# Performance work log

Measured on AMD Instinct MI355X. Metric: run time of the kernel, lower is better.

## Reference

```python
import jax, jax.numpy as jnp
import numpy as np
import math

EMB_DIM = 256
HEADS = 8
HEAD_DIM = EMB_DIM // HEADS
N_LAYERS = 6
GRID_H = 32
GRID_W = 32
SEQ = GRID_H * GRID_W
LN_EPS = 1e-5


def _layernorm(x, w, b):
    mu = jnp.mean(x, axis=-1, keepdims=True)
    var = jnp.mean(jnp.square(x - mu), axis=-1, keepdims=True)
    return (x - mu) * jax.lax.rsqrt(var + LN_EPS) * w + b


def _sinusoidal_table(num_pos, dim):
    inv_freq = 1.0 / (10000.0 ** (jnp.arange(0, dim, 2, dtype=jnp.float32) / dim))
    t = jnp.arange(num_pos, dtype=jnp.float32)
    sinusoid = t[:, None] * inv_freq[None, :]  # [P, dim/2]
    return jnp.concatenate([jnp.sin(sinusoid), jnp.cos(sinusoid)], axis=-1)  # [P, dim]


def _alibi_bias(num_heads, seq_len):
    # 2D Manhattan distances over the flattened grid (Two-slope-Alibi: factors = 1)
    xs, ys = jnp.meshgrid(jnp.arange(GRID_H), jnp.arange(GRID_W), indexing='ij')
    xf = xs.reshape(-1).astype(jnp.float32)
    yf = ys.reshape(-1).astype(jnp.float32)
    dist = jnp.abs(xf[:, None] - xf[None, :]) + jnp.abs(yf[:, None] - yf[None, :])
    dist = jnp.abs(dist[:seq_len, :seq_len])  # rpe_abs=True
    i = jnp.arange(num_heads, dtype=jnp.float32)
    slopes_l = -(2.0 ** (-(1.0 + i)))   # start_exponent=1, geometric ratio 1/2, times -1
    slopes_r = -(2.0 ** (-(0.5 + i)))   # start_exponent=0.5
    alibi_l = slopes_l[:, None, None] * dist[None]
    alibi_r = slopes_r[:, None, None] * dist[None]
    # triu + tril (diagonal dist = 0 so double-count is harmless)
    return jnp.triu(alibi_r) + jnp.tril(alibi_l)  # [H, S, S]


def reference(tokens, pos_ids, emb_table, input_weight, position_weight,
              ln1_w, ln1_b, ln2_w, ln2_b, w1, b1, w2, b2, lnf_w, lnf_b):
    B, S = tokens.shape
    # embeddings + sinusoidal positional embedding, mixed via weighted_sum_no_norm
    x_emb = emb_table[tokens]                                   # [B, S, D]
    pos_emb = _sinusoidal_table(SEQ, EMB_DIM)[pos_ids][None]    # [1, S, D]
    x = input_weight * x_emb + position_weight * pos_emb        # [B, S, D]

    bias = _alibi_bias(HEADS, S)[None]                          # [1, H, S, S]
    scale = 1.0 / math.sqrt(HEAD_DIM)

    for l in range(N_LAYERS):
        # --- attention: manual 2D-Alibi path (q = k = v = layernormed x; no projections) ---
        xn = _layernorm(x, ln1_w[l], ln1_b[l])
        qkv = xn.reshape(B, S, HEADS, HEAD_DIM).transpose(0, 2, 1, 3)  # [B, H, S, d]
        scores = jnp.einsum('bhsd,bhtd->bhst', qkv, qkv) * scale + bias
        attn = jax.nn.softmax(scores, axis=-1)
        out = jnp.einsum('bhst,bhtd->bhsd', attn, qkv)
        out = out.transpose(0, 2, 1, 3).reshape(B, S, EMB_DIM)
        x = x + out
        # --- MLP: Linear(D, 2*mlp_dim) -> GELU(exact) -> Linear(2*mlp_dim, D) ---
        xn = _layernorm(x, ln2_w[l], ln2_b[l])
        h = jax.nn.gelu(xn @ w1[l] + b1[l], approximate=False)
        x = x + (h @ w2[l] + b2[l])

    return _layernorm(x, lnf_w, lnf_b)


def setup_inputs() -> dict:
    key = jax.random.key(0)
    ks = jax.random.split(key, 8)
    B, S, D, L = 16, SEQ, EMB_DIM, N_LAYERS
    H2 = 2 * 512  # mlp hidden = mlp_dim * 2
    return {
        'tokens': jax.random.randint(ks[0], (B, S), 0, 16),
        'pos_ids': jnp.arange(S),
        'emb_table': jax.random.normal(ks[1], (16, D), dtype=jnp.float32),
        'input_weight': jnp.ones((1,), jnp.float32),
        'position_weight': jnp.ones((1,), jnp.float32),
        'ln1_w': jnp.ones((L, D), jnp.float32),
        'ln1_b': jnp.zeros((L, D), jnp.float32),
        'ln2_w': jnp.ones((L, D), jnp.float32),
        'ln2_b': jnp.zeros((L, D), jnp.float32),
        'w1': jax.random.normal(ks[2], (L, D, H2), dtype=jnp.float32) * (1.0 / np.sqrt(D)),
        'b1': jnp.zeros((L, H2), jnp.float32),
        'w2': jax.random.normal(ks[3], (L, H2, D), dtype=jnp.float32) * (1.0 / np.sqrt(H2)),
        'b2': jnp.zeros((L, D), jnp.float32),
        'lnf_w': jnp.ones((D,), jnp.float32),
        'lnf_b': jnp.zeros((D,), jnp.float32),
    }
```

## Files before the change

### kernel.cpp

```cpp
#include <hip/hip_runtime.h>
#include <hip/hip_bf16.h>
#include <math.h>

#define B_   16
#define S_   1024
#define D_   256
#define H_   8
#define HD_  32
#define L_   6
#define H2_  1024
#define LN_EPS 1e-5f
#define LOG2E_ 1.4426950408889634f
#define SCALE_ 0.17677669529663687f

typedef __attribute__((ext_vector_type(8))) short frag;
typedef __attribute__((ext_vector_type(4))) float f32x4;

#define MFMA(a, b, c) __builtin_amdgcn_mfma_f32_16x16x32_bf16((a), (b), (c), 0, 0, 0)

__device__ inline ushort bf16b(float f) {
    uint u = __builtin_bit_cast(uint, f);
    u += 0x7fff + ((u >> 16) & 1);
    return (ushort)(u >> 16);
}
__device__ inline uint cvt_pk_bf16(float lo, float hi) {
    uint r;
    asm("v_cvt_pk_bf16_f32 %0, %1, %2" : "=v"(r) : "v"(lo), "v"(hi));
    return r;
}
__device__ inline float exp2_raw(float x) {
    float r;
    asm("v_exp_f32 %0, %1" : "=v"(r) : "v"(x));
    return r;
}
__device__ __forceinline__ void gload16(const ushort* g, ushort* l) {
    __builtin_amdgcn_global_load_lds(
        (const __attribute__((address_space(1))) uint*)g,
        (__attribute__((address_space(3))) uint*)l, 16, 0, 0);
}

__global__ __launch_bounds__(256) void wtr_kernel(
    const float* __restrict__ in, ushort* __restrict__ out, int K, int N)
{
    __shared__ ushort Ts[32][36];
    in  += (size_t)blockIdx.z * K * N;
    out += (size_t)blockIdx.z * K * N;
    int n0 = blockIdx.x * 32, k0 = blockIdx.y * 32;
    int r = threadIdx.x >> 3, c4 = (threadIdx.x & 7) * 4;
    float4 f = *(const float4*)(in + (size_t)(k0 + r) * N + n0 + c4);
    Ts[r][c4 + 0] = bf16b(f.x);
    Ts[r][c4 + 1] = bf16b(f.y);
    Ts[r][c4 + 2] = bf16b(f.z);
    Ts[r][c4 + 3] = bf16b(f.w);
    __syncthreads();
    ushort4 o = { Ts[c4 + 0][r], Ts[c4 + 1][r], Ts[c4 + 2][r], Ts[c4 + 3][r] };
    *(ushort4*)(out + (size_t)(n0 + r) * K + k0 + c4) = o;
}

__global__ __launch_bounds__(256) void embed_kernel(
    const int* __restrict__ tokens, const int* __restrict__ pos_ids,
    const float* __restrict__ emb, const float* __restrict__ iwp,
    const float* __restrict__ pwp, float* __restrict__ X)
{
    int bs = blockIdx.x;
    int s = bs & (S_ - 1);
    int d = threadIdx.x;
    int tok = tokens[bs];
    float p = (float)pos_ids[s];
    int j = (d < 128) ? d : (d - 128);
    float invf = exp2f(-(float)j * (13.287712379549449f / 128.0f));
    float ang = p * invf;
    float pe = (d < 128) ? sinf(ang) : cosf(ang);
    X[(size_t)bs * D_ + d] = iwp[0] * emb[tok * D_ + d] + pwp[0] * pe;
}

template<int MODE>
__global__ __launch_bounds__(256) void ln_kernel(
    const float* __restrict__ X, const float* __restrict__ w,
    const float* __restrict__ b, void* __restrict__ outp)
{
    int row = blockIdx.x * 4 + (threadIdx.x >> 6);
    int lane = threadIdx.x & 63;
    const float4 v = *(const float4*)(X + (size_t)row * D_ + lane * 4);
    float s = v.x + v.y + v.z + v.w;
    #pragma unroll
    for (int m = 1; m < 64; m <<= 1) s += __shfl_xor(s, m, 64);
    float mu = s * (1.0f / 256.0f);
    float dx = v.x - mu, dy = v.y - mu, dz = v.z - mu, dw = v.w - mu;
    float vs = dx * dx + dy * dy + dz * dz + dw * dw;
    #pragma unroll
    for (int m = 1; m < 64; m <<= 1) vs += __shfl_xor(vs, m, 64);
    float inv = rsqrtf(vs * (1.0f / 256.0f) + LN_EPS);
    float4 wv = *(const float4*)(w + lane * 4);
    float4 bv = *(const float4*)(b + lane * 4);
    float o0 = dx * inv * wv.x + bv.x;
    float o1 = dy * inv * wv.y + bv.y;
    float o2 = dz * inv * wv.z + bv.z;
    float o3 = dw * inv * wv.w + bv.w;
    if constexpr (MODE == 0) {
        float4 o = { o0, o1, o2, o3 };
        *(float4*)((float*)outp + (size_t)row * D_ + lane * 4) = o;
    } else if constexpr (MODE == 1) {
        int bb = row >> 10, ss = row & 1023;
        int h = lane >> 3, dd = (lane & 7) * 4;
        ushort4 o = { bf16b(o0), bf16b(o1), bf16b(o2), bf16b(o3) };
        *(ushort4*)((ushort*)outp + (((size_t)(bb * H_ + h) * S_ + ss) * HD_ + dd)) = o;
    } else {
        ushort4 o = { bf16b(o0), bf16b(o1), bf16b(o2), bf16b(o3) };
        *(ushort4*)((ushort*)outp + (size_t)row * D_ + lane * 4) = o;
    }
}

__global__ __launch_bounds__(256) void vtr_kernel(
    const ushort* __restrict__ XNB, ushort* __restrict__ VTI)
{
    __shared__ ushort Ts[32][136];
    const int bh = blockIdx.y;
    const int sblk = blockIdx.x * 128;
    const ushort* __restrict__ base = XNB + (size_t)bh * (S_ * HD_);
    #pragma unroll
    for (int i = 0; i < 2; ++i) {
        int cid = i * 256 + threadIdx.x;
        int s = cid >> 2, c = cid & 3;
        uint4 u = *(const uint4*)(base + (size_t)(sblk + s) * HD_ + c * 8);
        int col = (s & ~63) + 32 * ((s >> 4) & 1) + 8 * ((s >> 2) & 3)
                + 4 * ((s >> 5) & 1) + (s & 3);
        int d0 = c * 8;
        Ts[d0 + 0][col] = (ushort)(u.x & 0xffff);
        Ts[d0 + 1][col] = (ushort)(u.x >> 16);
        Ts[d0 + 2][col] = (ushort)(u.y & 0xffff);
        Ts[d0 + 3][col] = (ushort)(u.y >> 16);
        Ts[d0 + 4][col] = (ushort)(u.z & 0xffff);
        Ts[d0 + 5][col] = (ushort)(u.z >> 16);
        Ts[d0 + 6][col] = (ushort)(u.w & 0xffff);
        Ts[d0 + 7][col] = (ushort)(u.w >> 16);
    }
    __syncthreads();
    #pragma unroll
    for (int i = 0; i < 2; ++i) {
        int cid = i * 256 + threadIdx.x;
        int d = cid >> 4, ch = cid & 15;
        uint4 o = *(const uint4*)&Ts[d][ch * 8];
        *(uint4*)(VTI + ((size_t)bh * HD_ + d) * S_ + sblk + ch * 8) = o;
    }
}

__global__ __launch_bounds__(256) void attn_kernel(
    const ushort* __restrict__ XNB, const ushort* __restrict__ VTI,
    float* __restrict__ X)
{
    const int bi = blockIdx.x;
    const int xcd = bi & 7, m = bi >> 3;
    const int bh = xcd * 16 + (m >> 3);
    const int bx = m & 7;
    const int b = bh >> 3, h = bh & 7;

    const ushort* __restrict__ base = XNB + (size_t)bh * (S_ * HD_);
    const ushort* __restrict__ vbase = VTI + (size_t)bh * (HD_ * S_);
    const int tid = threadIdx.x;
    const int w = tid >> 6, l = tid & 63, g = l >> 4, ll = l & 15;
    const int q0 = bx * 128 + w * 32;
    const int qgA = q0 + ll, qgB = q0 + 16 + ll;
    const int xq = q0 >> 5;
    const int yqA = ll, yqB = 16 + ll;

    const float C1 = SCALE_ * LOG2E_;
    frag qfA = *(const frag*)(base + (size_t)qgA * HD_ + g * 8);
    frag qfB = *(const frag*)(base + (size_t)qgB * HD_ + g * 8);
    #pragma unroll
    for (int i = 0; i < 8; ++i) {
        float fa = __builtin_bit_cast(float, ((uint)(ushort)qfA[i]) << 16);
        float fb = __builtin_bit_cast(float, ((uint)(ushort)qfB[i]) << 16);
        qfA[i] = (short)bf16b(fa * C1);
        qfB[i] = (short)bf16b(fb * C1);
    }

    const float slr = -exp2f(-(0.5f + (float)h)) * LOG2E_;
    const float sll = -exp2f(-(1.0f + (float)h)) * LOG2E_;
    const int itb = 2 * bx + (w >> 1);

    float dabs[4], d16m[4], d16p[4];
    #pragma unroll
    for (int r = 0; r < 4; ++r) {
        int del = ll - 4 * g - r;
        dabs[r] = (float)abs(del);
        d16m[r] = (float)(16 - del);
        d16p[r] = (float)(16 + del);
    }

    f32x4 o0A = {0,0,0,0}, o1A = {0,0,0,0}, osA = {0,0,0,0};
    f32x4 o0B = {0,0,0,0}, o1B = {0,0,0,0}, osB = {0,0,0,0};
    const f32x4 zc = {0,0,0,0};
    const short one_s = (short)0x3F80;
    const frag ones = { one_s, one_s, one_s, one_s, one_s, one_s, one_s, one_s };

    const ushort* kp  = base  + (size_t)ll * HD_ + g * 8;
    const ushort* vpa = vbase + (size_t)ll * S_ + g * 8;
    const ushort* vpb = vbase + (size_t)(16 + ll) * S_ + g * 8;

    frag Ka0, Ka1, Ka2, Ka3, Va0, Va1, Va2, Va3;
    frag Kb0, Kb1, Kb2, Kb3, Vb0, Vb1, Vb2, Vb3;

    Ka0 = *(const frag*)(kp);
    Ka1 = *(const frag*)(kp + 16 * HD_);
    Ka2 = *(const frag*)(kp + 32 * HD_);
    Ka3 = *(const frag*)(kp + 48 * HD_);
    Va0 = *(const frag*)(vpa);
    Va1 = *(const frag*)(vpb);
    Va2 = *(const frag*)(vpa + 32);
    Va3 = *(const frag*)(vpb + 32);
    kp += 64 * HD_; vpa += 64; vpb += 64;

#define EXACTR(r)                                                             \
  { int t0 = tb + 4 * g + (r);                                                \
    { int tg = t0;      int xt = tg >> 5, yt = tg & 31;                       \
      eA0[r] = exp2_raw(fmaf((tg > qgA) ? slr : sll,                          \
               (float)(abs(xq - xt) + abs(yqA - yt)), sa0[r]));               \
      eB0[r] = exp2_raw(fmaf((tg > qgB) ? slr : sll,                          \
               (float)(abs(xq - xt) + abs(yqB - yt)), sb0[r])); }             \
    { int tg = t0 + 16; int xt = tg >> 5, yt = tg & 31;                       \
      eA1[r] = exp2_raw(fmaf((tg > qgA) ? slr : sll,                          \
               (float)(abs(xq - xt) + abs(yqA - yt)), sa1[r]));               \
      eB1[r] = exp2_raw(fmaf((tg > qgB) ? slr : sll,                          \
               (float)(abs(xq - xt) + abs(yqB - yt)), sb1[r])); }             \
    { int tg = t0 + 32; int xt = tg >> 5, yt = tg & 31;                       \
      eA2[r] = exp2_raw(fmaf((tg > qgA) ? slr : sll,                          \
               (float)(abs(xq - xt) + abs(yqA - yt)), sa2[r]));               \
      eB2[r] = exp2_raw(fmaf((tg > qgB) ? slr : sll,                          \
               (float)(abs(xq - xt) + abs(yqB - yt)), sb2[r])); }             \
    { int tg = t0 + 48; int xt = tg >> 5, yt = tg & 31;                       \
      eA3[r] = exp2_raw(fmaf((tg > qgA) ? slr : sll,                          \
               (float)(abs(xq - xt) + abs(yqA - yt)), sa3[r]));               \
      eB3[r] = exp2_raw(fmaf((tg > qgB) ? slr : sll,                          \
               (float)(abs(xq - xt) + abs(yqB - yt)), sb3[r])); } }

#define FASTR(r)                                                              \
    eA0[r] = exp2_raw(fmaf(sl, dabs[r] + ax0, sa0[r]));                       \
    eA1[r] = exp2_raw(fmaf(sl, d16m[r] + ax0, sa1[r]));                       \
    eA2[r] = exp2_raw(fmaf(sl, dabs[r] + ax1, sa2[r]));                       \
    eA3[r] = exp2_raw(fmaf(sl, d16m[r] + ax1, sa3[r]));                       \
    eB0[r] = exp2_raw(fmaf(sl, d16p[r] + ax0, sb0[r]));                       \
    eB1[r] = exp2_raw(fmaf(sl, dabs[r] + ax0, sb1[r]));                       \
    eB2[r] = exp2_raw(fmaf(sl, d16p[r] + ax1, sb2[r]));                       \
    eB3[r] = exp2_raw(fmaf(sl, dabs[r] + ax1, sb3[r]));

#define STEP(IT, K0,K1,K2,K3, V0,V1,V2,V3, NK0,NK1,NK2,NK3, NV0,NV1,NV2,NV3) \
  { NK0 = *(const frag*)(kp);                                                 \
    NK1 = *(const frag*)(kp + 16 * HD_);                                      \
    NK2 = *(const frag*)(kp + 32 * HD_);                                      \
    NK3 = *(const frag*)(kp + 48 * HD_);                                      \
    NV0 = *(const frag*)(vpa);                                                \
    NV1 = *(const frag*)(vpb);                                                \
    NV2 = *(const frag*)(vpa + 32);                                           \
    NV3 = *(const frag*)(vpb + 32);                                           \
    kp += 64 * HD_; vpa += 64; vpb += 64;                                     \
    const int tb = (IT) * 64;                                                 \
    __builtin_amdgcn_s_setprio(1);                                            \
    f32x4 sa0 = MFMA(K0, qfA, zc);                                            \
    f32x4 sa1 = MFMA(K1, qfA, zc);                                            \
    f32x4 sa2 = MFMA(K2, qfA, zc);                                            \
    f32x4 sa3 = MFMA(K3, qfA, zc);                                            \
    f32x4 sb0 = MFMA(K0, qfB, zc);                                            \
    f32x4 sb1 = MFMA(K1, qfB, zc);                                            \
    f32x4 sb2 = MFMA(K2, qfB, zc);                                            \
    f32x4 sb3 = MFMA(K3, qfB, zc);                                            \
    __builtin_amdgcn_s_setprio(0);                                            \
    f32x4 eA0, eA1, eA2, eA3, eB0, eB1, eB2, eB3;                             \
    if ((IT) == itb) {                                                        \
        EXACTR(0) EXACTR(1) EXACTR(2) EXACTR(3)                               \
    } else {                                                                  \
        const float sl = ((IT) > itb) ? slr : sll;                            \
        const float ax0 = (float)abs(xq - 2 * (IT));                          \
        const float ax1 = (float)abs(xq - 2 * (IT) - 1);                      \
        FASTR(0) FASTR(1) FASTR(2) FASTR(3)                                   \
    }                                                                         \
    uint4 pa0 = { cvt_pk_bf16(eA0[0], eA0[1]), cvt_pk_bf16(eA0[2], eA0[3]),   \
                  cvt_pk_bf16(eA2[0], eA2[1]), cvt_pk_bf16(eA2[2], eA2[3]) }; \
    uint4 pa1 = { cvt_pk_bf16(eA1[0], eA1[1]), cvt_pk_bf16(eA1[2], eA1[3]),   \
                  cvt_pk_bf16(eA3[0], eA3[1]), cvt_pk_bf16(eA3[2], eA3[3]) }; \
    uint4 pb0 = { cvt_pk_bf16(eB0[0], eB0[1]), cvt_pk_bf16(eB0[2], eB0[3]),   \
                  cvt_pk_bf16(eB2[0], eB2[1]), cvt_pk_bf16(eB2[2], eB2[3]) }; \
    uint4 pb1 = { cvt_pk_bf16(eB1[0], eB1[1]), cvt_pk_bf16(eB1[2], eB1[3]),   \
                  cvt_pk_bf16(eB3[0], eB3[1]), cvt_pk_bf16(eB3[2], eB3[3]) }; \
    frag pfA0 = __builtin_bit_cast(frag, pa0);                                \
    frag pfA1 = __builtin_bit_cast(frag, pa1);                                \
    frag pfB0 = __builtin_bit_cast(frag, pb0);                                \
    frag pfB1 = __builtin_bit_cast(frag, pb1);                                \
    __builtin_amdgcn_s_setprio(1);                                            \
    o0A = MFMA(pfA0, V0, o0A);  o1A = MFMA(pfA0, V1, o1A);                    \
    osA = MFMA(pfA0, ones, osA);                                              \
    o0A = MFMA(pfA1, V2, o0A);  o1A = MFMA(pfA1, V3, o1A);                    \
    osA = MFMA(pfA1, ones, osA);                                              \
    o0B = MFMA(pfB0, V0, o0B);  o1B = MFMA(pfB0, V1, o1B);                    \
    osB = MFMA(pfB0, ones, osB);                                              \
    o0B = MFMA(pfB1, V2, o0B);  o1B = MFMA(pfB1, V3, o1B);                    \
    osB = MFMA(pfB1, ones, osB);                                              \
    __builtin_amdgcn_s_setprio(0);                                            \
  }

    for (int it2 = 0; it2 < 16; it2 += 2) {
        STEP(it2,     Ka0,Ka1,Ka2,Ka3, Va0,Va1,Va2,Va3,
                      Kb0,Kb1,Kb2,Kb3, Vb0,Vb1,Vb2,Vb3)
        STEP(it2 + 1, Kb0,Kb1,Kb2,Kb3, Vb0,Vb1,Vb2,Vb3,
                      Ka0,Ka1,Ka2,Ka3, Va0,Va1,Va2,Va3)
    }
#undef STEP
#undef FASTR
#undef EXACTR

    #pragma unroll
    for (int r = 0; r < 4; ++r) {
        float invA = 1.0f / osA[r];
        float invB = 1.0f / osB[r];
        float* xpA = X + ((size_t)(b * S_ + q0 + g * 4 + r)) * D_ + h * HD_;
        float* xpB = X + ((size_t)(b * S_ + q0 + 16 + g * 4 + r)) * D_ + h * HD_;
        xpA[ll]      += o0A[r] * invA;
        xpA[16 + ll] += o1A[r] * invA;
        xpB[ll]      += o0B[r] * invB;
        xpB[16 + ll] += o1B[r] * invB;
    }
}

__global__ __launch_bounds__(256) void gemm1_kernel(
    const ushort* __restrict__ A, const ushort* __restrict__ Bt,
    const float* __restrict__ bias, ushort* __restrict__ Hout)
{
    __shared__ ushort As[128 * 32];
    __shared__ ushort Bs[128 * 32];
    const int tid = threadIdx.x;
    const int w = tid >> 6, l = tid & 63, g = l >> 4, ll = l & 15;
    const int wm = w >> 1, wn = w & 1;
    const int row0 = blockIdx.y * 128, col0 = blockIdx.x * 128;

    const int srow = w * 32 + (l >> 2);
    const int scol = (l & 3) * 8;
    const ushort* ga = A  + (size_t)(row0 + srow) * 256 + scol;
    const ushort* gb = Bt + (size_t)(col0 + srow) * 256 + scol;
    ushort* lA = &As[w * 1024 + l * 8];
    ushort* lB = &Bs[w * 1024 + l * 8];

    f32x4 acc[4][4] = {};
    for (int k0 = 0; k0 < 256; k0 += 32) {
        __syncthreads();
        gload16(ga + k0,            lA);
        gload16(ga + k0 + 16 * 256, lA + 512);
        gload16(gb + k0,            lB);
        gload16(gb + k0 + 16 * 256, lB + 512);
        __syncthreads();
        frag af[4], bfr[4];
        #pragma unroll
        for (int mb = 0; mb < 4; ++mb)
            af[mb] = *(const frag*)&As[(wm * 64 + mb * 16 + ll) * 32 + g * 8];
        #pragma unroll
        for (int nb = 0; nb < 4; ++nb)
            bfr[nb] = *(const frag*)&Bs[(wn * 64 + nb * 16 + ll) * 32 + g * 8];
        #pragma unroll
        for (int mb = 0; mb < 4; ++mb)
            #pragma unroll
            for (int nb = 0; nb < 4; ++nb)
                acc[mb][nb] = MFMA(af[mb], bfr[nb], acc[mb][nb]);
    }

    #pragma unroll
    for (int nb = 0; nb < 4; ++nb) {
        int col = col0 + wn * 64 + nb * 16 + ll;
        float bv = bias[col];
        #pragma unroll
        for (int mb = 0; mb < 4; ++mb) {
            #pragma unroll
            for (int r = 0; r < 4; ++r) {
                int row = row0 + wm * 64 + mb * 16 + g * 4 + r;
                float v = acc[mb][nb][r] + bv;
                float u2 = 1.5957691216f * v + 0.0713548162f * (v * v * v);
                float e = exp2_raw(u2 * LOG2E_);
                float rr = __builtin_amdgcn_rcpf(e + 1.0f);
                float gl = v - v * rr;
                Hout[(size_t)row * 1024 + col] = bf16b(gl);
            }
        }
    }
}

__global__ __launch_bounds__(256) void gemm2_kernel(
    const ushort* __restrict__ A, const ushort* __restrict__ Bt,
    const float* __restrict__ bias, float* __restrict__ X)
{
    __shared__ ushort As[128 * 32];
    __shared__ ushort Bs[64 * 32];
    const int tid = threadIdx.x;
    const int w = tid >> 6, l = tid & 63, g = l >> 4, ll = l & 15;
    const int row0 = blockIdx.y * 128, col0 = blockIdx.x * 64;

    const int srow = w * 32 + (l >> 2);
    const int scol = (l & 3) * 8;
    const ushort* ga = A  + (size_t)(row0 + srow) * 1024 + scol;
    const ushort* gb = Bt + (size_t)(col0 + w * 16 + (l >> 2)) * 1024 + scol;
    ushort* lA = &As[w * 1024 + l * 8];
    ushort* lB = &Bs[w * 512 + l * 8];

    f32x4 acc[2][4] = {};
    for (int k0 = 0; k0 < 1024; k0 += 32) {
        __syncthreads();
        gload16(ga + k0,             lA);
        gload16(ga + k0 + 16 * 1024, lA + 512);
        gload16(gb + k0,             lB);
        __syncthreads();
        frag af[2], bfr[4];
        #pragma unroll
        for (int mb = 0; mb < 2; ++mb)
            af[mb] = *(const frag*)&As[(w * 32 + mb * 16 + ll) * 32 + g * 8];
        #pragma unroll
        for (int nb = 0; nb < 4; ++nb)
            bfr[nb] = *(const frag*)&Bs[(nb * 16 + ll) * 32 + g * 8];
        #pragma unroll
        for (int mb = 0; mb < 2; ++mb)
            #pragma unroll
            for (int nb = 0; nb < 4; ++nb)
                acc[mb][nb] = MFMA(af[mb], bfr[nb], acc[mb][nb]);
    }

    #pragma unroll
    for (int nb = 0; nb < 4; ++nb) {
        int col = col0 + nb * 16 + ll;
        float bv = bias[col];
        #pragma unroll
        for (int mb = 0; mb < 2; ++mb) {
            #pragma unroll
            for (int r = 0; r < 4; ++r) {
                int row = row0 + w * 32 + mb * 16 + g * 4 + r;
                float* xp = X + (size_t)row * 256 + col;
                *xp += acc[mb][nb][r] + bv;
            }
        }
    }
}

extern "C" void kernel_launch(void* const* d_in, const int* in_sizes, int n_in,
                              void* d_out, int out_size, void* d_ws, size_t ws_size,
                              hipStream_t stream)
{
    const int*   tokens  = (const int*)d_in[0];
    const int*   pos_ids = (const int*)d_in[1];
    const float* emb     = (const float*)d_in[2];
    const float* iw      = (const float*)d_in[3];
    const float* pw      = (const float*)d_in[4];
    const float* ln1w    = (const float*)d_in[5];
    const float* ln1b    = (const float*)d_in[6];
    const float* ln2w    = (const float*)d_in[7];
    const float* ln2b    = (const float*)d_in[8];
    const float* w1      = (const float*)d_in[9];
    const float* b1      = (const float*)d_in[10];
    const float* w2      = (const float*)d_in[11];
    const float* b2      = (const float*)d_in[12];
    const float* lnfw    = (const float*)d_in[13];
    const float* lnfb    = (const float*)d_in[14];

    float* x = (float*)d_out;
    char* ws = (char*)d_ws;
    ushort* xn   = (ushort*)ws;
    ushort* vti  = (ushort*)(ws + 8388608);
    ushort* hbuf = (ushort*)(ws + 16777216);
    ushort* w1t  = (ushort*)(ws + 50331648);
    ushort* w2t  = (ushort*)(ws + 53477376);

    wtr_kernel<<<dim3(32, 8, L_), 256, 0, stream>>>(w1, w1t, 256, 1024);
    wtr_kernel<<<dim3(8, 32, L_), 256, 0, stream>>>(w2, w2t, 1024, 256);

    embed_kernel<<<B_ * S_, 256, 0, stream>>>(tokens, pos_ids, emb, iw, pw, x);

    for (int l = 0; l < L_; l++) {
        ln_kernel<1><<<(B_ * S_) / 4, 256, 0, stream>>>(x, ln1w + l * D_, ln1b + l * D_, xn);
        vtr_kernel<<<dim3(S_ / 128, B_ * H_), 256, 0, stream>>>(xn, vti);
        attn_kernel<<<(S_ / 128) * B_ * H_, 256, 0, stream>>>(xn, vti, x);
        ln_kernel<2><<<(B_ * S_) / 4, 256, 0, stream>>>(x, ln2w + l * D_, ln2b + l * D_, xn);
        gemm1_kernel<<<dim3(H2_ / 128, (B_ * S_) / 128), 256, 0, stream>>>(
            xn, w1t + (size_t)l * D_ * H2_, b1 + (size_t)l * H2_, hbuf);
        gemm2_kernel<<<dim3(D_ / 64, (B_ * S_) / 128), 256, 0, stream>>>(
            hbuf, w2t + (size_t)l * H2_ * D_, b2 + (size_t)l * D_, x);
    }
    ln_kernel<0><<<(B_ * S_) / 4, 256, 0, stream>>>(x, lnfw, lnfb, x);
}
```

Before: 730.6 us.

## Stage attention K/V tiles through double-buffered LDS instead of per-wave global loads

The attention kernel now cooperatively loads each 64-key K and V tile into double-buffered shared memory, using async global-to-LDS copies (gload16), and each wave reads its fragments from LDS. Before, every wave loaded the same K/V fragments straight from global memory into registers. The aim is to cut redundant global/L2 traffic, since four waves share one tile. The cost is a block-wide barrier every iteration, and the s_setprio hints around the MFMAs are dropped. gload16 is assumed to be defined in the part of the file not shown.

```diff
diff --git a/kernel.cpp b/kernel.cpp
--- a/kernel.cpp
+++ b/kernel.cpp
@@ -149,6 +149,9 @@
     const ushort* __restrict__ XNB, const ushort* __restrict__ VTI,
     float* __restrict__ X)
 {
+    __shared__ ushort Kl[2][2048];
+    __shared__ ushort Vl[2][2048];
+
     const int bi = blockIdx.x;
     const int xcd = bi & 7, m = bi >> 3;
     const int bh = xcd * 16 + (m >> 3);
@@ -194,22 +197,16 @@
     const short one_s = (short)0x3F80;
     const frag ones = { one_s, one_s, one_s, one_s, one_s, one_s, one_s, one_s };
 
-    const ushort* kp  = base  + (size_t)ll * HD_ + g * 8;
-    const ushort* vpa = vbase + (size_t)ll * S_ + g * 8;
-    const ushort* vpb = vbase + (size_t)(16 + ll) * S_ + g * 8;
-
-    frag Ka0, Ka1, Ka2, Ka3, Va0, Va1, Va2, Va3;
-    frag Kb0, Kb1, Kb2, Kb3, Vb0, Vb1, Vb2, Vb3;
-
-    Ka0 = *(const frag*)(kp);
-    Ka1 = *(const frag*)(kp + 16 * HD_);
-    Ka2 = *(const frag*)(kp + 32 * HD_);
-    Ka3 = *(const frag*)(kp + 48 * HD_);
-    Va0 = *(const frag*)(vpa);
-    Va1 = *(const frag*)(vpb);
-    Va2 = *(const frag*)(vpa + 32);
-    Va3 = *(const frag*)(vpb + 32);
-    kp += 64 * HD_; vpa += 64; vpb += 64;
+    const ushort* ksrc = base  + (size_t)(16 * w + ll) * HD_ + g * 8;
+    const ushort* vsrc = vbase + (size_t)((w >> 1) * 16 + ll) * S_ + (w & 1) * 32 + g * 8;
+    const int dst = (w * 64 + l) * 8;
+
+#define STAGE(NB, TILE)                                                       \
+    gload16(ksrc + (size_t)(TILE) * 64 * HD_, &Kl[NB][dst]);                  \
+    gload16(vsrc + (TILE) * 64,               &Vl[NB][dst]);
+
+    STAGE(0, 0)
+    __syncthreads();
 
 #define EXACTR(r)                                                             \
   { int t0 = tb + 4 * g + (r);                                                \
@@ -244,67 +241,63 @@
     eB2[r] = exp2_raw(fmaf(sl, d16p[r] + ax1, sb2[r]));                       \
     eB3[r] = exp2_raw(fmaf(sl, dabs[r] + ax1, sb3[r]));
 
-#define STEP(IT, K0,K1,K2,K3, V0,V1,V2,V3, NK0,NK1,NK2,NK3, NV0,NV1,NV2,NV3) \
-  { NK0 = *(const frag*)(kp);                                                 \
-    NK1 = *(const frag*)(kp + 16 * HD_);                                      \
-    NK2 = *(const frag*)(kp + 32 * HD_);                                      \
-    NK3 = *(const frag*)(kp + 48 * HD_);                                      \
-    NV0 = *(const frag*)(vpa);                                                \
-    NV1 = *(const frag*)(vpb);                                                \
-    NV2 = *(const frag*)(vpa + 32);                                           \
-    NV3 = *(const frag*)(vpb + 32);                                           \
-    kp += 64 * HD_; vpa += 64; vpb += 64;                                     \
-    const int tb = (IT) * 64;                                                 \
-    __builtin_amdgcn_s_setprio(1);                                            \
-    f32x4 sa0 = MFMA(K0, qfA, zc);                                            \
-    f32x4 sa1 = MFMA(K1, qfA, zc);                                            \
-    f32x4 sa2 = MFMA(K2, qfA, zc);                                            \
-    f32x4 sa3 = MFMA(K3, qfA, zc);                                            \
-    f32x4 sb0 = MFMA(K0, qfB, zc);                                            \
-    f32x4 sb1 = MFMA(K1, qfB, zc);                                            \
-    f32x4 sb2 = MFMA(K2, qfB, zc);                                            \
-    f32x4 sb3 = MFMA(K3, qfB, zc);                                            \
-    __builtin_amdgcn_s_setprio(0);                                            \
-    f32x4 eA0, eA1, eA2, eA3, eB0, eB1, eB2, eB3;                             \
-    if ((IT) == itb) {                                                        \
-        EXACTR(0) EXACTR(1) EXACTR(2) EXACTR(3)                               \
-    } else {                                                                  \
-        const float sl = ((IT) > itb) ? slr : sll;                            \
-        const float ax0 = (float)abs(xq - 2 * (IT));                          \
-        const float ax1 = (float)abs(xq - 2 * (IT) - 1);                      \
-        FASTR(0) FASTR(1) FASTR(2) FASTR(3)                                   \
-    }                                                                         \
-    uint4 pa0 = { cvt_pk_bf16(eA0[0], eA0[1]), cvt_pk_bf16(eA0[2], eA0[3]),   \
-                  cvt_pk_bf16(eA2[0], eA2[1]), cvt_pk_bf16(eA2[2], eA2[3]) }; \
-    uint4 pa1 = { cvt_pk_bf16(eA1[0], eA1[1]), cvt_pk_bf16(eA1[2], eA1[3]),   \
-                  cvt_pk_bf16(eA3[0], eA3[1]), cvt_pk_bf16(eA3[2], eA3[3]) }; \
-    uint4 pb0 = { cvt_pk_bf16(eB0[0], eB0[1]), cvt_pk_bf16(eB0[2], eB0[3]),   \
-                  cvt_pk_bf16(eB2[0], eB2[1]), cvt_pk_bf16(eB2[2], eB2[3]) }; \
-    uint4 pb1 = { cvt_pk_bf16(eB1[0], eB1[1]), cvt_pk_bf16(eB1[2], eB1[3]),   \
-                  cvt_pk_bf16(eB3[0], eB3[1]), cvt_pk_bf16(eB3[2], eB3[3]) }; \
-    frag pfA0 = __builtin_bit_cast(frag, pa0);                                \
-    frag pfA1 = __builtin_bit_cast(frag, pa1);                                \
-    frag pfB0 = __builtin_bit_cast(frag, pb0);                                \
-    frag pfB1 = __builtin_bit_cast(frag, pb1);                                \
-    __builtin_amdgcn_s_setprio(1);                                            \
-    o0A = MFMA(pfA0, V0, o0A);  o1A = MFMA(pfA0, V1, o1A);                    \
-    osA = MFMA(pfA0, ones, osA);                                              \
-    o0A = MFMA(pfA1, V2, o0A);  o1A = MFMA(pfA1, V3, o1A);                    \
-    osA = MFMA(pfA1, ones, osA);                                              \
-    o0B = MFMA(pfB0, V0, o0B);  o1B = MFMA(pfB0, V1, o1B);                    \
-    osB = MFMA(pfB0, ones, osB);                                              \
-    o0B = MFMA(pfB1, V2, o0B);  o1B = MFMA(pfB1, V3, o1B);                    \
-    osB = MFMA(pfB1, ones, osB);                                              \
-    __builtin_amdgcn_s_setprio(0);                                            \
-  }
-
-    for (int it2 = 0; it2 < 16; it2 += 2) {
-        STEP(it2,     Ka0,Ka1,Ka2,Ka3, Va0,Va1,Va2,Va3,
-                      Kb0,Kb1,Kb2,Kb3, Vb0,Vb1,Vb2,Vb3)
-        STEP(it2 + 1, Kb0,Kb1,Kb2,Kb3, Vb0,Vb1,Vb2,Vb3,
-                      Ka0,Ka1,Ka2,Ka3, Va0,Va1,Va2,Va3)
-    }
-#undef STEP
+    for (int it = 0; it < 16; ++it) {
+        const int cur = it & 1, nxt = cur ^ 1;
+        const int tb = it * 64;
+        STAGE(nxt, (it + 1) & 15)
+
+        frag K0 = *(const frag*)&Kl[cur][l * 8];
+        frag K1 = *(const frag*)&Kl[cur][512 + l * 8];
+        frag K2 = *(const frag*)&Kl[cur][1024 + l * 8];
+        frag K3 = *(const frag*)&Kl[cur][1536 + l * 8];
+        frag V0 = *(const frag*)&Vl[cur][l * 8];
+        frag V2 = *(const frag*)&Vl[cur][512 + l * 8];
+        frag V1 = *(const frag*)&Vl[cur][1024 + l * 8];
+        frag V3 = *(const frag*)&Vl[cur][1536 + l * 8];
+
+        f32x4 sa0 = MFMA(K0, qfA, zc);
+        f32x4 sa1 = MFMA(K1, qfA, zc);
+        f32x4 sa2 = MFMA(K2, qfA, zc);
+        f32x4 sa3 = MFMA(K3, qfA, zc);
+        f32x4 sb0 = MFMA(K0, qfB, zc);
+        f32x4 sb1 = MFMA(K1, qfB, zc);
+        f32x4 sb2 = MFMA(K2, qfB, zc);
+        f32x4 sb3 = MFMA(K3, qfB, zc);
+
+        f32x4 eA0, eA1, eA2, eA3, eB0, eB1, eB2, eB3;
+        if (it == itb) {
+            EXACTR(0) EXACTR(1) EXACTR(2) EXACTR(3)
+        } else {
+            const float sl = (it > itb) ? slr : sll;
+            const float ax0 = (float)abs(xq - 2 * it);
+            const float ax1 = (float)abs(xq - 2 * it - 1);
+            FASTR(0) FASTR(1) FASTR(2) FASTR(3)
+        }
+        uint4 pa0 = { cvt_pk_bf16(eA0[0], eA0[1]), cvt_pk_bf16(eA0[2], eA0[3]),
+                      cvt_pk_bf16(eA2[0], eA2[1]), cvt_pk_bf16(eA2[2], eA2[3]) };
+        uint4 pa1 = { cvt_pk_bf16(eA1[0], eA1[1]), cvt_pk_bf16(eA1[2], eA1[3]),
+                      cvt_pk_bf16(eA3[0], eA3[1]), cvt_pk_bf16(eA3[2], eA3[3]) };
+        uint4 pb0 = { cvt_pk_bf16(eB0[0], eB0[1]), cvt_pk_bf16(eB0[2], eB0[3]),
+                      cvt_pk_bf16(eB2[0], eB2[1]), cvt_pk_bf16(eB2[2], eB2[3]) };
+        uint4 pb1 = { cvt_pk_bf16(eB1[0], eB1[1]), cvt_pk_bf16(eB1[2], eB1[3]),
+                      cvt_pk_bf16(eB3[0], eB3[1]), cvt_pk_bf16(eB3[2], eB3[3]) };
+        frag pfA0 = __builtin_bit_cast(frag, pa0);
+        frag pfA1 = __builtin_bit_cast(frag, pa1);
+        frag pfB0 = __builtin_bit_cast(frag, pb0);
+        frag pfB1 = __builtin_bit_cast(frag, pb1);
+
+        o0A = MFMA(pfA0, V0, o0A);  o1A = MFMA(pfA0, V1, o1A);
+        osA = MFMA(pfA0, ones, osA);
+        o0A = MFMA(pfA1, V2, o0A);  o1A = MFMA(pfA1, V3, o1A);
+        osA = MFMA(pfA1, ones, osA);
+        o0B = MFMA(pfB0, V0, o0B);  o1B = MFMA(pfB0, V1, o1B);
+        osB = MFMA(pfB0, ones, osB);
+        o0B = MFMA(pfB1, V2, o0B);  o1B = MFMA(pfB1, V3, o1B);
+        osB = MFMA(pfB1, ones, osB);
+
+        __syncthreads();
+    }
+#undef STAGE
 #undef FASTR
 #undef EXACTR
 
```

Result: faster. 679.3 us (-7.0%).

## Stage K/V tiles through LDS triple buffer and software-pipeline QK with PV

Applied to the files above, without the earlier changes.

Replaces per-wave direct global loads of K and V fragments with cooperative async global-to-LDS loads into a three-slot ring buffer, synchronised with waitcnt and barriers. Each wave now loads one quarter of each tile instead of every wave loading the whole tile, removing redundant global traffic across the four waves. The loop is also restructured so the next tile's QK MFMAs are issued alongside the current tile's PV MFMAs, with the exp computation moved after them, so matrix and vector work can overlap. It adds a block-wide barrier every tile, LDS usage that may lower occupancy, and extra register pressure from carrying scores across iterations. The final round stages a tile index that wraps to 0 and is never used, wasting a small load.

```diff
diff --git a/kernel.cpp b/kernel.cpp
--- a/kernel.cpp
+++ b/kernel.cpp
@@ -149,6 +149,9 @@
     const ushort* __restrict__ XNB, const ushort* __restrict__ VTI,
     float* __restrict__ X)
 {
+    __shared__ ushort Kl[3][2048];
+    __shared__ ushort Vl[3][2048];
+
     const int bi = blockIdx.x;
     const int xcd = bi & 7, m = bi >> 3;
     const int bh = xcd * 16 + (m >> 3);
@@ -194,25 +197,19 @@
     const short one_s = (short)0x3F80;
     const frag ones = { one_s, one_s, one_s, one_s, one_s, one_s, one_s, one_s };
 
-    const ushort* kp  = base  + (size_t)ll * HD_ + g * 8;
-    const ushort* vpa = vbase + (size_t)ll * S_ + g * 8;
-    const ushort* vpb = vbase + (size_t)(16 + ll) * S_ + g * 8;
-
-    frag Ka0, Ka1, Ka2, Ka3, Va0, Va1, Va2, Va3;
-    frag Kb0, Kb1, Kb2, Kb3, Vb0, Vb1, Vb2, Vb3;
-
-    Ka0 = *(const frag*)(kp);
-    Ka1 = *(const frag*)(kp + 16 * HD_);
-    Ka2 = *(const frag*)(kp + 32 * HD_);
-    Ka3 = *(const frag*)(kp + 48 * HD_);
-    Va0 = *(const frag*)(vpa);
-    Va1 = *(const frag*)(vpb);
-    Va2 = *(const frag*)(vpa + 32);
-    Va3 = *(const frag*)(vpb + 32);
-    kp += 64 * HD_; vpa += 64; vpb += 64;
-
-#define EXACTR(r)                                                             \
-  { int t0 = tb + 4 * g + (r);                                                \
+    const ushort* ksrc = base  + (size_t)(16 * w + ll) * HD_ + g * 8;
+    const ushort* vsrc = vbase + (size_t)((w >> 1) * 16 + ll) * S_ + (w & 1) * 32 + g * 8;
+    const int dst = (w * 64 + l) * 8;
+
+#define STAGE(NB, TILE)                                                       \
+    gload16(ksrc + (size_t)((TILE) & 15) * 64 * HD_, &Kl[NB][dst]);           \
+    gload16(vsrc + (((TILE) & 15) * 64),             &Vl[NB][dst]);
+
+    f32x4 sa0, sa1, sa2, sa3, sb0, sb1, sb2, sb3;
+    frag pfA0, pfA1, pfB0, pfB1;
+
+#define EXACTR(r, TB)                                                         \
+  { int t0 = (TB) + 4 * g + (r);                                              \
     { int tg = t0;      int xt = tg >> 5, yt = tg & 31;                       \
       eA0[r] = exp2_raw(fmaf((tg > qgA) ? slr : sll,                          \
                (float)(abs(xq - xt) + abs(yqA - yt)), sa0[r]));               \
@@ -244,30 +241,11 @@
     eB2[r] = exp2_raw(fmaf(sl, d16p[r] + ax1, sb2[r]));                       \
     eB3[r] = exp2_raw(fmaf(sl, dabs[r] + ax1, sb3[r]));
 
-#define STEP(IT, K0,K1,K2,K3, V0,V1,V2,V3, NK0,NK1,NK2,NK3, NV0,NV1,NV2,NV3) \
-  { NK0 = *(const frag*)(kp);                                                 \
-    NK1 = *(const frag*)(kp + 16 * HD_);                                      \
-    NK2 = *(const frag*)(kp + 32 * HD_);                                      \
-    NK3 = *(const frag*)(kp + 48 * HD_);                                      \
-    NV0 = *(const frag*)(vpa);                                                \
-    NV1 = *(const frag*)(vpb);                                                \
-    NV2 = *(const frag*)(vpa + 32);                                           \
-    NV3 = *(const frag*)(vpb + 32);                                           \
-    kp += 64 * HD_; vpa += 64; vpb += 64;                                     \
-    const int tb = (IT) * 64;                                                 \
-    __builtin_amdgcn_s_setprio(1);                                            \
-    f32x4 sa0 = MFMA(K0, qfA, zc);                                            \
-    f32x4 sa1 = MFMA(K1, qfA, zc);                                            \
-    f32x4 sa2 = MFMA(K2, qfA, zc);                                            \
-    f32x4 sa3 = MFMA(K3, qfA, zc);                                            \
-    f32x4 sb0 = MFMA(K0, qfB, zc);                                            \
-    f32x4 sb1 = MFMA(K1, qfB, zc);                                            \
-    f32x4 sb2 = MFMA(K2, qfB, zc);                                            \
-    f32x4 sb3 = MFMA(K3, qfB, zc);                                            \
-    __builtin_amdgcn_s_setprio(0);                                            \
-    f32x4 eA0, eA1, eA2, eA3, eB0, eB1, eB2, eB3;                             \
+#define COMPUTE_E(IT)                                                         \
+  { f32x4 eA0, eA1, eA2, eA3, eB0, eB1, eB2, eB3;                             \
     if ((IT) == itb) {                                                        \
-        EXACTR(0) EXACTR(1) EXACTR(2) EXACTR(3)                               \
+        const int tb_ = (IT) * 64;                                            \
+        EXACTR(0, tb_) EXACTR(1, tb_) EXACTR(2, tb_) EXACTR(3, tb_)           \
     } else {                                                                  \
         const float sl = ((IT) > itb) ? slr : sll;                            \
         const float ax0 = (float)abs(xq - 2 * (IT));                          \
@@ -282,11 +260,51 @@
                   cvt_pk_bf16(eB2[0], eB2[1]), cvt_pk_bf16(eB2[2], eB2[3]) }; \
     uint4 pb1 = { cvt_pk_bf16(eB1[0], eB1[1]), cvt_pk_bf16(eB1[2], eB1[3]),   \
                   cvt_pk_bf16(eB3[0], eB3[1]), cvt_pk_bf16(eB3[2], eB3[3]) }; \
-    frag pfA0 = __builtin_bit_cast(frag, pa0);                                \
-    frag pfA1 = __builtin_bit_cast(frag, pa1);                                \
-    frag pfB0 = __builtin_bit_cast(frag, pb0);                                \
-    frag pfB1 = __builtin_bit_cast(frag, pb1);                                \
+    pfA0 = __builtin_bit_cast(frag, pa0);                                     \
+    pfA1 = __builtin_bit_cast(frag, pa1);                                     \
+    pfB0 = __builtin_bit_cast(frag, pb0);                                     \
+    pfB1 = __builtin_bit_cast(frag, pb1);                                     \
+  }
+
+    STAGE(0, 0)
+    STAGE(1, 1)
+    asm volatile("s_waitcnt vmcnt(2)" ::: "memory");
+    __builtin_amdgcn_s_barrier();
+    __builtin_amdgcn_sched_barrier(0);
+    {
+        frag K0 = *(const frag*)&Kl[0][l * 8];
+        frag K1 = *(const frag*)&Kl[0][512 + l * 8];
+        frag K2 = *(const frag*)&Kl[0][1024 + l * 8];
+        frag K3 = *(const frag*)&Kl[0][1536 + l * 8];
+        sa0 = MFMA(K0, qfA, zc); sa1 = MFMA(K1, qfA, zc);
+        sa2 = MFMA(K2, qfA, zc); sa3 = MFMA(K3, qfA, zc);
+        sb0 = MFMA(K0, qfB, zc); sb1 = MFMA(K1, qfB, zc);
+        sb2 = MFMA(K2, qfB, zc); sb3 = MFMA(K3, qfB, zc);
+        COMPUTE_E(0)
+    }
+
+#define ROUND(T, BC, BN, BS)                                                  \
+  { asm volatile("s_waitcnt vmcnt(0)" ::: "memory");     \
+    __builtin_amdgcn_s_barrier();                                             \
+    __builtin_amdgcn_sched_barrier(0);                                        \
+    STAGE(BS, (T) + 2)                                                        \
+    frag K0 = *(const frag*)&Kl[BN][l * 8];                                   \
+    frag K1 = *(const frag*)&Kl[BN][512 + l * 8];                             \
+    frag K2 = *(const frag*)&Kl[BN][1024 + l * 8];                            \
+    frag K3 = *(const frag*)&Kl[BN][1536 + l * 8];                            \
+    frag V0 = *(const frag*)&Vl[BC][l * 8];                                   \
+    frag V2 = *(const frag*)&Vl[BC][512 + l * 8];                             \
+    frag V1 = *(const frag*)&Vl[BC][1024 + l * 8];                            \
+    frag V3 = *(const frag*)&Vl[BC][1536 + l * 8];                            \
     __builtin_amdgcn_s_setprio(1);                                            \
+    f32x4 na0 = MFMA(K0, qfA, zc);                                            \
+    f32x4 na1 = MFMA(K1, qfA, zc);                                            \
+    f32x4 na2 = MFMA(K2, qfA, zc);                                            \
+    f32x4 na3 = MFMA(K3, qfA, zc);                                            \
+    f32x4 nb0 = MFMA(K0, qfB, zc);                                            \
+    f32x4 nb1 = MFMA(K1, qfB, zc);                                            \
+    f32x4 nb2 = MFMA(K2, qfB, zc);                                            \
+    f32x4 nb3 = MFMA(K3, qfB, zc);                                            \
     o0A = MFMA(pfA0, V0, o0A);  o1A = MFMA(pfA0, V1, o1A);                    \
     osA = MFMA(pfA0, ones, osA);                                              \
     o0A = MFMA(pfA1, V2, o0A);  o1A = MFMA(pfA1, V3, o1A);                    \
@@ -296,17 +314,22 @@
     o0B = MFMA(pfB1, V2, o0B);  o1B = MFMA(pfB1, V3, o1B);                    \
     osB = MFMA(pfB1, ones, osB);                                              \
     __builtin_amdgcn_s_setprio(0);                                            \
+    sa0 = na0; sa1 = na1; sa2 = na2; sa3 = na3;                               \
+    sb0 = nb0; sb1 = nb1; sb2 = nb2; sb3 = nb3;                               \
+    COMPUTE_E((T) + 1)                                                        \
   }
 
-    for (int it2 = 0; it2 < 16; it2 += 2) {
-        STEP(it2,     Ka0,Ka1,Ka2,Ka3, Va0,Va1,Va2,Va3,
-                      Kb0,Kb1,Kb2,Kb3, Vb0,Vb1,Vb2,Vb3)
-        STEP(it2 + 1, Kb0,Kb1,Kb2,Kb3, Vb0,Vb1,Vb2,Vb3,
-                      Ka0,Ka1,Ka2,Ka3, Va0,Va1,Va2,Va3)
-    }
-#undef STEP
+    ROUND(0,  0, 1, 2)  ROUND(1,  1, 2, 0)  ROUND(2,  2, 0, 1)
+    ROUND(3,  0, 1, 2)  ROUND(4,  1, 2, 0)  ROUND(5,  2, 0, 1)
+    ROUND(6,  0, 1, 2)  ROUND(7,  1, 2, 0)  ROUND(8,  2, 0, 1)
+    ROUND(9,  0, 1, 2)  ROUND(10, 1, 2, 0)  ROUND(11, 2, 0, 1)
+    ROUND(12, 0, 1, 2)  ROUND(13, 1, 2, 0)  ROUND(14, 2, 0, 1)
+    ROUND(15, 0, 1, 2)
+#undef ROUND
+#undef COMPUTE_E
 #undef FASTR
 #undef EXACTR
+#undef STAGE
 
     #pragma unroll
     for (int r = 0; r < 4; ++r) {
```

After: 692.8 us. -5.2%, faster.
